# Performance work log

Measured on AMD Instinct MI355X. Metric: run time of the kernel, lower is better.

## Reference

```python
import jax, jax.numpy as jnp
import numpy as np

MUL = 16                                   # multiplicity of each irrep block
N_EDGES = 200_000
INV_SQRT3 = float(1.0 / np.sqrt(3.0))      # wigner-3j values: w3j(1,1,0)=delta/sqrt(3), etc.
# e3nn normalization (irrep_normalization='component', path_normalization='element'):
# path_weight = sqrt(dim(out_irrep) / fan_in), fan_in = sum of mul_in1*mul_in2 over paths
# sharing the same output. Both 0e and 1o outputs have two paths with fan 16 each -> fan_in=32.
PW0 = float(np.sqrt(1.0 / (2 * MUL)))      # output 0e (dim 1)
PW1 = float(np.sqrt(3.0 / (2 * MUL)))      # output 1o (dim 3)


def setup_inputs() -> dict:
    key = jax.random.key(0)
    k1, k2, k3 = jax.random.split(key, 3)
    u = jax.random.normal(k1, (N_EDGES, 4 * MUL), jnp.float32)       # 16x0e + 16x1o -> 64
    v = jax.random.normal(k2, (N_EDGES, 4), jnp.float32)             # 1x0e + 1x1o -> 4
    weight = jax.random.normal(k3, (N_EDGES, 4 * MUL * MUL), jnp.float32)  # 4 uvw paths
    return {"u": u, "v": v, "weight": weight}


def reference(u, v, weight):
    N = u.shape[0]
    u0 = u[:, :MUL]                          # [N,16] scalar (0e) channels
    u1 = u[:, MUL:].reshape(N, MUL, 3)       # [N,16,3] vector (1o) channels
    v0 = v[:, 0]                             # [N] sh 0e
    v1 = v[:, 1:4]                           # [N,3] sh 1o
    w = weight.reshape(N, 4, MUL, MUL)       # path order: (0e,0e->0e),(0e,1o->1o),(1o,0e->1o),(1o,1o->0e)
    w1, w2, w3, w4 = w[:, 0], w[:, 1], w[:, 2], w[:, 3]

    # ---- 0e output: paths 1 and 4 ----
    s1 = u0 * v0[:, None]                                   # [N,16], CG = 1
    s4 = jnp.einsum('nuk,nk->nu', u1, v1) * INV_SQRT3       # [N,16], CG = delta_ij/sqrt(3)
    out0 = PW0 * (jnp.einsum('nuw,nu->nw', w1, s1)
                  + jnp.einsum('nuw,nu->nw', w4, s4))       # [N,16]

    # ---- 1o output: paths 2 and 3 ----
    t2 = u0[:, :, None] * v1[:, None, :] * INV_SQRT3        # [N,16,3]
    t3 = u1 * (v0[:, None, None] * INV_SQRT3)               # [N,16,3]
    out1 = PW1 * (jnp.einsum('nuw,nuk->nwk', w2, t2)
                  + jnp.einsum('nuw,nuk->nwk', w3, t3))     # [N,16,3]

    return jnp.concatenate([out0, out1.reshape(N, 3 * MUL)], axis=1)  # [N,64]
```

## Files before the change

### kernel.cpp

```cpp
#include <hip/hip_runtime.h>


#define WAVE 64

__global__ __launch_bounds__(256) void fctp_kernel(
    const float* __restrict__ u,
    const float* __restrict__ v,
    const float* __restrict__ wgt,
    float* __restrict__ out,
    int N)
{
    constexpr float INV_SQRT3 = 0.57735026918962576451f;
    constexpr float PW0 = 0.17677669529663688110f;
    constexpr float PW1 = 0.30618621784789726f;

    const int lane = threadIdx.x & 63;
    const int wv   = threadIdx.x >> 6;
    int n = blockIdx.x * 4 + wv;
    if (n >= N) n = N - 1;

    __shared__ float sh[4][84];
    float* s = sh[wv];

    s[lane] = u[(size_t)n * 64 + lane];
    if (lane < 4) s[80 + lane] = v[(size_t)n * 4 + lane];
    __syncthreads();

    if (lane < 16) {
        const int b = 16 + 3 * lane;
        float d = s[b] * s[81] + s[b + 1] * s[82] + s[b + 2] * s[83];
        s[64 + lane] = d;
    }
    __syncthreads();

    const bool is0 = (lane < 16);
    const int  o    = lane - 16;
    const int  wcol = is0 ? lane : (o / 3);
    const int  k    = is0 ? 0    : (o - 3 * wcol);
    const float v0  = s[80];
    const float p   = is0 ? v0        : s[81 + k] * INV_SQRT3;
    const float q   = is0 ? INV_SQRT3 : v0 * INV_SQRT3;
    const int offA = is0 ? wcol         : (256 + wcol);
    const int offB = is0 ? (768 + wcol) : (512 + wcol);
    const int offY  = is0 ? 64 : (16 + k);
    const int ystep = is0 ? 1 : 3;

    const float* wp = wgt + (size_t)n * 1024;

    float acc = 0.0f;
#pragma unroll
    for (int uu = 0; uu < 16; ++uu) {
        const float X  = s[uu];
        const float Y  = s[offY + uu * ystep];
        const float wa = wp[offA + uu * 16];
        const float wb = wp[offB + uu * 16];
        acc = fmaf(wa, X * p, acc);
        acc = fmaf(wb, Y * q, acc);
    }

    out[(size_t)n * 64 + lane] = (is0 ? PW0 : PW1) * acc;
}

extern "C" void kernel_launch(void* const* d_in, const int* in_sizes, int n_in,
                              void* d_out, int out_size, void* d_ws, size_t ws_size,
                              hipStream_t stream)
{
    const float* u   = (const float*)d_in[0];
    const float* v   = (const float*)d_in[1];
    const float* wgt = (const float*)d_in[2];
    float* out = (float*)d_out;

    const int N = in_sizes[1] / 4;
    const int blocks = (N + 3) / 4;
    fctp_kernel<<<blocks, 256, 0, stream>>>(u, v, wgt, out, N);
}
```

Measured before the change: 158.7 us.

## Parallelize over input channel with float4 weight loads and DPP row reductions

Each lane now owns one input channel u and a group of four output columns, loading the weights as float4 vectors instead of strided scalar loads. Partial products are summed across the 16 lanes of each row with DPP row-rotate adds, and lanes then select their output element from the reduced values. This removes the shared-memory staging and both __syncthreads, and widens the weight loads, which dominate memory traffic. In exchange it adds 20 four-step DPP reductions per lane and a scattered output index mapping.

```diff
diff --git a/kernel.cpp b/kernel.cpp
--- a/kernel.cpp
+++ b/kernel.cpp
@@ -1,12 +1,29 @@
 #include <hip/hip_runtime.h>
 
 
-#define WAVE 64
+template <int CTRL>
+__device__ __forceinline__ float row_rot_add(float x) {
+    int t = __builtin_amdgcn_update_dpp(0, __float_as_int(x), CTRL, 0xF, 0xF, false);
+    return x + __int_as_float(t);
+}
+__device__ __forceinline__ float rowsum16(float x) {
+    x = row_rot_add<0x128>(x);
+    x = row_rot_add<0x124>(x);
+    x = row_rot_add<0x122>(x);
+    x = row_rot_add<0x121>(x);
+    return x;
+}
+__device__ __forceinline__ float sel4(float a, float b, float c, float d, int i) {
+    float r = (i == 1) ? b : a;
+    r = (i == 2) ? c : r;
+    r = (i == 3) ? d : r;
+    return r;
+}
 
 __global__ __launch_bounds__(256) void fctp_kernel(
-    const float* __restrict__ u,
-    const float* __restrict__ v,
-    const float* __restrict__ wgt,
+    const float* __restrict__ U,
+    const float* __restrict__ V,
+    const float* __restrict__ W,
     float* __restrict__ out,
     int N)
 {
@@ -19,58 +36,77 @@
     int n = blockIdx.x * 4 + wv;
     if (n >= N) n = N - 1;
 
-    __shared__ float sh[4][84];
-    float* s = sh[wv];
+    const int u = lane & 15;
+    const int c = lane >> 4;
 
-    s[lane] = u[(size_t)n * 64 + lane];
-    if (lane < 4) s[80 + lane] = v[(size_t)n * 4 + lane];
-    __syncthreads();
+    const float4* wq = (const float4*)(W + (size_t)n * 1024);
+    const int fi = u * 4 + c;
+    const float4 L1 = wq[  0 + fi];
+    const float4 L2 = wq[ 64 + fi];
+    const float4 L3 = wq[128 + fi];
+    const float4 L4 = wq[192 + fi];
 
-    if (lane < 16) {
-        const int b = 16 + 3 * lane;
-        float d = s[b] * s[81] + s[b + 1] * s[82] + s[b + 2] * s[83];
-        s[64 + lane] = d;
+    const float4 vv = ((const float4*)V)[n];
+    const float v0 = vv.x;
+    const float* up = U + (size_t)n * 64;
+    const float u0  = up[u];
+    const float u10 = up[16 + 3 * u + 0];
+    const float u11 = up[16 + 3 * u + 1];
+    const float u12 = up[16 + 3 * u + 2];
+    const float d4  = u10 * vv.y + u11 * vv.z + u12 * vv.w;
+
+    const float a1 = u0 * v0;
+    const float a4 = d4 * INV_SQRT3;
+
+    float p0x = L1.x * a1 + L4.x * a4;
+    float p0y = L1.y * a1 + L4.y * a4;
+    float p0z = L1.z * a1 + L4.z * a4;
+    float p0w = L1.w * a1 + L4.w * a4;
+
+    float pa0 = L2.x * u0, pa1 = L2.y * u0, pa2 = L2.z * u0, pa3 = L2.w * u0;
+
+    float b00 = L3.x * u10, b01 = L3.y * u10, b02 = L3.z * u10, b03 = L3.w * u10;
+    float b10 = L3.x * u11, b11 = L3.y * u11, b12 = L3.z * u11, b13 = L3.w * u11;
+    float b20 = L3.x * u12, b21 = L3.y * u12, b22 = L3.z * u12, b23 = L3.w * u12;
+
+    p0x = rowsum16(p0x); p0y = rowsum16(p0y); p0z = rowsum16(p0z); p0w = rowsum16(p0w);
+    pa0 = rowsum16(pa0); pa1 = rowsum16(pa1); pa2 = rowsum16(pa2); pa3 = rowsum16(pa3);
+    b00 = rowsum16(b00); b01 = rowsum16(b01); b02 = rowsum16(b02); b03 = rowsum16(b03);
+    b10 = rowsum16(b10); b11 = rowsum16(b11); b12 = rowsum16(b12); b13 = rowsum16(b13);
+    b20 = rowsum16(b20); b21 = rowsum16(b21); b22 = rowsum16(b22); b23 = rowsum16(b23);
+
+    float val;
+    int oidx;
+    if (u < 4) {
+        float r = sel4(p0x, p0y, p0z, p0w, u);
+        val  = PW0 * r;
+        oidx = 4 * c + u;
+    } else {
+        const int j = u - 4;
+        const int i = (j * 11) >> 5;
+        const int k = j - 3 * i;
+        const float ra  = sel4(pa0, pa1, pa2, pa3, i);
+        const float vk  = (k == 0) ? vv.y : (k == 1) ? vv.z : vv.w;
+        const float rb0 = sel4(b00, b01, b02, b03, i);
+        const float rb1 = sel4(b10, b11, b12, b13, i);
+        const float rb2 = sel4(b20, b21, b22, b23, i);
+        const float rb  = (k == 0) ? rb0 : (k == 1) ? rb1 : rb2;
+        val  = PW1 * INV_SQRT3 * (ra * vk + v0 * rb);
+        oidx = 16 + 12 * c + j;
     }
-    __syncthreads();
-
-    const bool is0 = (lane < 16);
-    const int  o    = lane - 16;
-    const int  wcol = is0 ? lane : (o / 3);
-    const int  k    = is0 ? 0    : (o - 3 * wcol);
-    const float v0  = s[80];
-    const float p   = is0 ? v0        : s[81 + k] * INV_SQRT3;
-    const float q   = is0 ? INV_SQRT3 : v0 * INV_SQRT3;
-    const int offA = is0 ? wcol         : (256 + wcol);
-    const int offB = is0 ? (768 + wcol) : (512 + wcol);
-    const int offY  = is0 ? 64 : (16 + k);
-    const int ystep = is0 ? 1 : 3;
-
-    const float* wp = wgt + (size_t)n * 1024;
-
-    float acc = 0.0f;
-#pragma unroll
-    for (int uu = 0; uu < 16; ++uu) {
-        const float X  = s[uu];
-        const float Y  = s[offY + uu * ystep];
-        const float wa = wp[offA + uu * 16];
-        const float wb = wp[offB + uu * 16];
-        acc = fmaf(wa, X * p, acc);
-        acc = fmaf(wb, Y * q, acc);
-    }
-
-    out[(size_t)n * 64 + lane] = (is0 ? PW0 : PW1) * acc;
+    out[(size_t)n * 64 + oidx] = val;
 }
 
 extern "C" void kernel_launch(void* const* d_in, const int* in_sizes, int n_in,
                               void* d_out, int out_size, void* d_ws, size_t ws_size,
                               hipStream_t stream)
 {
-    const float* u   = (const float*)d_in[0];
-    const float* v   = (const float*)d_in[1];
-    const float* wgt = (const float*)d_in[2];
+    const float* U = (const float*)d_in[0];
+    const float* V = (const float*)d_in[1];
+    const float* W = (const float*)d_in[2];
     float* out = (float*)d_out;
 
     const int N = in_sizes[1] / 4;
     const int blocks = (N + 3) / 4;
-    fctp_kernel<<<blocks, 256, 0, stream>>>(u, v, wgt, out, N);
+    fctp_kernel<<<blocks, 256, 0, stream>>>(U, V, W, out, N);
 }
```

After: 164.9 us. +3.9%, slower.
